# Kernel tuning notes

Measured on AMD Instinct MI355X. Metric: run time of the kernel, lower is better.

The kernel has to match this reference:

```python
import jax, jax.numpy as jnp
import numpy as np

R_MAX = 32
S_MAX = 2
C_Z = 128
IN_DIM = 4 * R_MAX + 2 * S_MAX + 7  # 139
N = 1024


def setup_inputs() -> dict:
    key = jax.random.key(0)
    k1, k2, k3, k4, k5, k6 = jax.random.split(key, 6)
    return {
        "asym_id": jax.random.randint(k1, (N,), 0, 8, dtype=jnp.int64 if jax.config.jax_enable_x64 else jnp.int32),
        "residue_index": jax.random.randint(k2, (N,), 0, 512),
        "entity_id": jax.random.randint(k3, (N,), 0, 4),
        "token_index": jax.random.randint(k4, (N,), 0, 2048),
        "sym_id": jax.random.randint(k5, (N,), 0, 4),
        "weight": jax.random.normal(k6, (C_Z, IN_DIM), dtype=jnp.float32),
    }


def reference(asym_id, residue_index, entity_id, token_index, sym_id, weight):
    r_max, s_max = R_MAX, S_MAX
    pos_dim = 2 * r_max + 2    # 66
    token_dim = 2 * r_max + 2  # 66
    # Pre-projected one-hot rows -> lookup tables (original casts to fp16, accumulates fp32)
    w16 = weight.astype(jnp.float16)
    W_pos = w16[:, :pos_dim].T                                # [66, c_z]
    W_token = w16[:, pos_dim:pos_dim + token_dim].T            # [66, c_z]
    W_entity = w16[:, pos_dim + token_dim]                     # [c_z]
    W_chain = w16[:, pos_dim + token_dim + 1:].T               # [6, c_z]

    same_chain = asym_id[:, None] == asym_id[None, :]          # [N, N]
    same_res = residue_index[:, None] == residue_index[None, :]
    same_ent = entity_id[:, None] == entity_id[None, :]

    d_res = jnp.clip(residue_index[:, None] - residue_index[None, :] + r_max, 0, 2 * r_max)
    d_res = jnp.where(same_chain, d_res, 2 * r_max + 1)

    d_tok = jnp.clip(token_index[:, None] - token_index[None, :] + r_max, 0, 2 * r_max)
    d_tok = jnp.where(same_chain & same_res, d_tok, 2 * r_max + 1)

    d_ch = jnp.clip(sym_id[:, None] - sym_id[None, :] + s_max, 0, 2 * s_max)
    d_ch = jnp.where(same_ent, d_ch, 2 * s_max + 1)

    out = (
        W_pos[d_res].astype(jnp.float32)
        + W_token[d_tok].astype(jnp.float32)
        + W_chain[d_ch].astype(jnp.float32)
        + jnp.where(same_ent[:, :, None], W_entity.astype(jnp.float32)[None, None, :], 0.0)
    )  # [N, N, c_z] fp32
    return out
```

## Files before the change

### kernel.cpp

```cpp
#include <hip/hip_runtime.h>
#include <hip/hip_fp16.h>

constexpr int NN    = 1024;
constexpr int CZ    = 128;
constexpr int INDIM = 139;

typedef float f4 __attribute__((ext_vector_type(4)));


__global__ __launch_bounds__(256, 2) void relpos_kernel(
    const int* __restrict__ asym, const int* __restrict__ resi,
    const int* __restrict__ ent,  const int* __restrict__ tok,
    const int* __restrict__ sym,  const float* __restrict__ weight,
    float* __restrict__ out)
{
    __shared__ float lds[18432];
    float* P = lds;
    float* T = lds + 8448;
    float* C = lds + 16896;

    const int tid = threadIdx.x;

    for (int idx = tid; idx < 8448; idx += 256) {
        const int d = idx >> 7, c = idx & 127;
        P[idx] = __half2float(__float2half(weight[c * INDIM + d]));
        T[idx] = __half2float(__float2half(weight[c * INDIM + 66 + d]));
    }
    for (int idx = tid; idx < 768; idx += 256) {
        const int d = idx >> 7, c = idx & 127;
        const float ch = __half2float(__float2half(weight[c * INDIM + 133 + d]));
        const float en = __half2float(__float2half(weight[c * INDIM + 132]));
        C[idx]       = ch;
        C[768 + idx] = ch + en;
    }
    __syncthreads();

    const int bid   = blockIdx.x;
    const int i     = bid >> 1;
    const int jbase = (bid & 1) << 9;

    const int ai = asym[i], ri = resi[i], ei = ent[i], ti = tok[i], si = sym[i];

    const int g  = tid >> 5;
    const int c4 = (tid & 31) << 2;

    float* const out_row = out + ((size_t)i * NN) * CZ + c4;

    #pragma unroll 4
    for (int jt = 0; jt < 64; ++jt) {
        const int j  = jbase + jt * 8 + g;
        const int aj = asym[j], rj = resi[j], ej = ent[j], tj = tok[j], sj = sym[j];

        const bool sc = (ai == aj);
        const bool sr = (ri == rj);
        const int  se = (ei == ej) ? 1 : 0;

        int dres = min(max(ri - rj + 32, 0), 64);
        if (!sc) dres = 65;
        int dtok = min(max(ti - tj + 32, 0), 64);
        if (!(sc && sr)) dtok = 65;
        int dch = min(max(si - sj + 2, 0), 4);
        if (!se) dch = 5;

        const f4 p  = *(const f4*)&P[dres * 128 + c4];
        const f4 t  = *(const f4*)&T[dtok * 128 + c4];
        const f4 cc = *(const f4*)&C[se * 768 + dch * 128 + c4];

        f4 o = p + t + cc;

        __builtin_nontemporal_store(o, (f4*)(out_row + (size_t)j * CZ));
    }
}

extern "C" void kernel_launch(void* const* d_in, const int* in_sizes, int n_in,
                              void* d_out, int out_size, void* d_ws, size_t ws_size,
                              hipStream_t stream) {
    const int*   asym   = (const int*)d_in[0];
    const int*   resi   = (const int*)d_in[1];
    const int*   ent    = (const int*)d_in[2];
    const int*   tok    = (const int*)d_in[3];
    const int*   sym    = (const int*)d_in[4];
    const float* weight = (const float*)d_in[5];
    float*       out    = (float*)d_out;

    relpos_kernel<<<NN * 2, 256, 0, stream>>>(asym, resi, ent, tok, sym, weight, out);
}
```

Baseline: 545.8 us.

## Precompute fp16-rounded tables and packed attributes in a prep kernel

Adds a small prep kernel that builds the fp16-rounded lookup tables and bit-packs the five per-token attributes into one word, storing both in workspace. The main kernel then fills LDS with contiguous vector copies instead of doing a strided, converting gather of the weights in every block, and stages the packed column attributes in LDS so each iteration needs one LDS read instead of five global loads. The packing masks assume the value ranges of the inputs (asym<8, ent/sym<4, resi<1024, tok<4096), and the change adds a second kernel launch.

```diff
diff --git a/kernel.cpp b/kernel.cpp
--- a/kernel.cpp
+++ b/kernel.cpp
@@ -7,49 +7,75 @@
 
 typedef float f4 __attribute__((ext_vector_type(4)));
 
+constexpr int TBL_FLOATS = 18432;
+constexpr int TBL_BYTES  = TBL_FLOATS * 4;
 
-__global__ __launch_bounds__(256, 2) void relpos_kernel(
-    const int* __restrict__ asym, const int* __restrict__ resi,
-    const int* __restrict__ ent,  const int* __restrict__ tok,
-    const int* __restrict__ sym,  const float* __restrict__ weight,
+__global__ void build_tables(const int* __restrict__ asym, const int* __restrict__ resi,
+                             const int* __restrict__ ent,  const int* __restrict__ tok,
+                             const int* __restrict__ sym,  const float* __restrict__ w,
+                             float* __restrict__ tbl, unsigned* __restrict__ packed)
+{
+    const int gtid   = blockIdx.x * 256 + threadIdx.x;
+    const int stride = gridDim.x * 256;
+
+    for (int idx = gtid; idx < 8448; idx += stride) {
+        const int d = idx >> 7, c = idx & 127;
+        tbl[idx]        = __half2float(__float2half(w[c * INDIM + d]));
+        tbl[8448 + idx] = __half2float(__float2half(w[c * INDIM + 66 + d]));
+    }
+    for (int idx = gtid; idx < 768; idx += stride) {
+        const int d = idx >> 7, c = idx & 127;
+        const float ch = __half2float(__float2half(w[c * INDIM + 133 + d]));
+        const float en = __half2float(__float2half(w[c * INDIM + 132]));
+        tbl[16896 + idx]       = ch;
+        tbl[16896 + 768 + idx] = ch + en;
+    }
+    for (int j = gtid; j < NN; j += stride) {
+        packed[j] = (unsigned)(asym[j] & 7)
+                  | ((unsigned)(ent[j]  & 3)    << 3)
+                  | ((unsigned)(sym[j]  & 3)    << 5)
+                  | ((unsigned)(resi[j] & 1023) << 7)
+                  | ((unsigned)(tok[j]  & 4095) << 17);
+    }
+}
+
+__global__ __launch_bounds__(256, 2) void relpos_main(
+    const float* __restrict__ tbl, const unsigned* __restrict__ packed,
     float* __restrict__ out)
 {
-    __shared__ float lds[18432];
-    float* P = lds;
-    float* T = lds + 8448;
-    float* C = lds + 16896;
+    __shared__ __attribute__((aligned(16))) float    lds[TBL_FLOATS];
+    __shared__ __attribute__((aligned(16))) unsigned attrs[512];
 
     const int tid = threadIdx.x;
 
-    for (int idx = tid; idx < 8448; idx += 256) {
-        const int d = idx >> 7, c = idx & 127;
-        P[idx] = __half2float(__float2half(weight[c * INDIM + d]));
-        T[idx] = __half2float(__float2half(weight[c * INDIM + 66 + d]));
+    {
+        const f4* __restrict__ src = (const f4*)tbl;
+        f4* __restrict__ dst = (f4*)lds;
+        #pragma unroll
+        for (int k = 0; k < 18; ++k) dst[tid + 256 * k] = src[tid + 256 * k];
     }
-    for (int idx = tid; idx < 768; idx += 256) {
-        const int d = idx >> 7, c = idx & 127;
-        const float ch = __half2float(__float2half(weight[c * INDIM + 133 + d]));
-        const float en = __half2float(__float2half(weight[c * INDIM + 132]));
-        C[idx]       = ch;
-        C[768 + idx] = ch + en;
-    }
-    __syncthreads();
 
     const int bid   = blockIdx.x;
     const int i     = bid >> 1;
     const int jbase = (bid & 1) << 9;
 
-    const int ai = asym[i], ri = resi[i], ei = ent[i], ti = tok[i], si = sym[i];
+    for (int k = tid; k < 512; k += 256) attrs[k] = packed[jbase + k];
+    __syncthreads();
+
+    const unsigned pi = packed[i];
+    const int ai = pi & 7, ei = (pi >> 3) & 3, si = (pi >> 5) & 3;
+    const int ri = (pi >> 7) & 1023, ti = (pi >> 17) & 4095;
 
     const int g  = tid >> 5;
     const int c4 = (tid & 31) << 2;
 
-    float* const out_row = out + ((size_t)i * NN) * CZ + c4;
+    float* outp = out + ((size_t)i << 17) + (size_t)(jbase + g) * CZ + c4;
 
     #pragma unroll 4
     for (int jt = 0; jt < 64; ++jt) {
-        const int j  = jbase + jt * 8 + g;
-        const int aj = asym[j], rj = resi[j], ej = ent[j], tj = tok[j], sj = sym[j];
+        const unsigned pj = attrs[jt * 8 + g];
+        const int aj = pj & 7, ej = (pj >> 3) & 3, sj = (pj >> 5) & 3;
+        const int rj = (pj >> 7) & 1023, tj = (pj >> 17) & 4095;
 
         const bool sc = (ai == aj);
         const bool sr = (ri == rj);
@@ -62,13 +88,12 @@
         int dch = min(max(si - sj + 2, 0), 4);
         if (!se) dch = 5;
 
-        const f4 p  = *(const f4*)&P[dres * 128 + c4];
-        const f4 t  = *(const f4*)&T[dtok * 128 + c4];
-        const f4 cc = *(const f4*)&C[se * 768 + dch * 128 + c4];
+        const f4 p  = *(const f4*)&lds[dres * 128 + c4];
+        const f4 t  = *(const f4*)&lds[8448 + dtok * 128 + c4];
+        const f4 cc = *(const f4*)&lds[16896 + se * 768 + dch * 128 + c4];
 
-        f4 o = p + t + cc;
-
-        __builtin_nontemporal_store(o, (f4*)(out_row + (size_t)j * CZ));
+        __builtin_nontemporal_store(p + t + cc, (f4*)outp);
+        outp += 8 * CZ;
     }
 }
 
@@ -83,5 +108,9 @@
     const float* weight = (const float*)d_in[5];
     float*       out    = (float*)d_out;
 
-    relpos_kernel<<<NN * 2, 256, 0, stream>>>(asym, resi, ent, tok, sym, weight, out);
+    float*    tbl    = (float*)d_ws;
+    unsigned* packed = (unsigned*)((char*)d_ws + TBL_BYTES);
+
+    build_tables<<<16, 256, 0, stream>>>(asym, resi, ent, tok, sym, weight, tbl, packed);
+    relpos_main<<<NN * 2, 256, 0, stream>>>(tbl, packed, out);
 }
```

Measured after the change: 530.7 us. 1.03x faster.
